# Kernel tuning notes

Measured on AMD Instinct MI355X. Metric: run time of the kernel, lower is better.

The kernel has to match this reference:

```python
import jax, jax.numpy as jnp
import numpy as np

B, S, D_IN, D_OUT, H = 2, 2048, 1024, 1024, 16
HD = D_OUT // H  # head dim = 64


def setup_inputs() -> dict:
    key = jax.random.key(0)
    ks = jax.random.split(key, 9)
    s_in = 1.0 / np.sqrt(D_IN)
    s_out = 1.0 / np.sqrt(D_OUT)
    return {
        "X": jax.random.normal(ks[0], (B, S, D_IN), dtype=jnp.float32),
        "Wq": jax.random.uniform(ks[1], (D_OUT, D_IN), jnp.float32, -s_in, s_in),
        "bq": jax.random.uniform(ks[2], (D_OUT,), jnp.float32, -s_in, s_in),
        "Wk": jax.random.uniform(ks[3], (D_OUT, D_IN), jnp.float32, -s_in, s_in),
        "bk": jax.random.uniform(ks[4], (D_OUT,), jnp.float32, -s_in, s_in),
        "Wv": jax.random.uniform(ks[5], (D_OUT, D_IN), jnp.float32, -s_in, s_in),
        "bv": jax.random.uniform(ks[6], (D_OUT,), jnp.float32, -s_in, s_in),
        "Wo": jax.random.uniform(ks[7], (D_OUT, D_OUT), jnp.float32, -s_out, s_out),
        "bo": jax.random.uniform(ks[8], (D_OUT,), jnp.float32, -s_out, s_out),
    }


def reference(X, Wq, bq, Wk, bk, Wv, bv, Wo, bo):
    scale = jnp.asarray(HD ** 0.5, X.dtype)  # self.dim = sqrt(head_dim)
    q = X @ Wq.T + bq  # [B,S,D_OUT]
    k = X @ Wk.T + bk
    v = X @ Wv.T + bv
    # split heads: b s (h d) -> b h s d
    q = q.reshape(B, S, H, HD).transpose(0, 2, 1, 3)
    k = k.reshape(B, S, H, HD).transpose(0, 2, 1, 3)
    v = v.reshape(B, S, H, HD).transpose(0, 2, 1, 3)
    scores = jnp.einsum('bhsd,bhtd->bhst', q, k) / scale  # [B,H,S,S]
    causal = jnp.triu(jnp.ones((S, S), dtype=bool), k=1)
    scores = jnp.where(causal, -jnp.inf, scores)
    weights = jax.nn.softmax(scores, axis=-1)
    out = jnp.einsum('bhst,bhtd->bhsd', weights, v)  # [B,H,S,HD]
    out = out.transpose(0, 2, 1, 3).reshape(B, S, D_OUT)  # b h s d -> b s (h d)
    return out @ Wo.T + bo
```

## Files before the change

### kernel.cpp

```cpp
#include <hip/hip_runtime.h>
#include <hip/hip_bf16.h>

typedef __bf16 bf16_t;
typedef __bf16 bf16x8 __attribute__((ext_vector_type(8)));
typedef float  f32x4  __attribute__((ext_vector_type(4)));
typedef unsigned short ushort_t;

#define MFMA16(a, b, c) __builtin_amdgcn_mfma_f32_16x16x32_bf16((a), (b), (c), 0, 0, 0)
#define GLDS16(g, l) __builtin_amdgcn_global_load_lds( \
    (const __attribute__((address_space(1))) unsigned int*)(g), \
    (__attribute__((address_space(3))) unsigned int*)(l), 16, 0, 0)

#define WAITCNT_VM(n)  (0x0F70 | (n))
#define WAITCNT_LGKM0  0xC07F

#define MEMFENCE asm volatile("" ::: "memory")

#define QSCALE 0.18033688f

__global__ __launch_bounds__(256) void cvt_all(
    const void* __restrict__ X,  const void* __restrict__ W0, const void* __restrict__ W1,
    const void* __restrict__ W2, const void* __restrict__ W3,
    const void* __restrict__ c0, const void* __restrict__ c1,
    const void* __restrict__ c2, const void* __restrict__ c3,
    bf16_t* __restrict__ Xb, bf16_t* __restrict__ Wb, float* __restrict__ biasF,
    int* __restrict__ flag)
{
    const int tid  = threadIdx.x;
    const int lane = tid & 63;
    const ushort_t u = ((const ushort_t*)X)[2 * lane];
    const int e = (u >> 7) & 0xFF;
    const int f = (__ballot(e >= 0xA0) != 0ull) ? 1 : 0;

    const int bid = blockIdx.x;
    if (bid >= 4096) {
        if (bid == 4096 && tid == 0) *flag = f;
        const int idx = ((bid - 4096) * 256 + tid) * 8;
        const int w = idx >> 10, off = idx & 1023;
        const void* src = (w == 0) ? c0 : (w == 1) ? c1 : (w == 2) ? c2 : c3;
        #pragma unroll
        for (int r = 0; r < 8; ++r)
            biasF[idx + r] = f ? ((const float*)src)[off + r]
                               : (float)((const bf16_t*)src)[off + r];
        return;
    }

    const long long i = (long long)bid * 2048 + tid * 8;
    const void* src;
    bf16_t* dst;
    long long off;
    if (i < 4194304) { src = X; dst = Xb; off = i; }
    else {
        const int w = (int)((i - 4194304) >> 20);
        off = (i - 4194304) & 1048575;
        src = (w == 0) ? W0 : (w == 1) ? W1 : (w == 2) ? W2 : W3;
        dst = Wb + (size_t)w * 1048576;
    }
    if (f) {
        const float* s = (const float*)src + off;
        const float4 a = *(const float4*)(s);
        const float4 b = *(const float4*)(s + 4);
        bf16x8 o;
        o[0] = (bf16_t)a.x; o[1] = (bf16_t)a.y; o[2] = (bf16_t)a.z; o[3] = (bf16_t)a.w;
        o[4] = (bf16_t)b.x; o[5] = (bf16_t)b.y; o[6] = (bf16_t)b.z; o[7] = (bf16_t)b.w;
        *(bf16x8*)(dst + off) = o;
    } else {
        *(bf16x8*)(dst + off) = *(const bf16x8*)((const bf16_t*)src + off);
    }
}

__global__ __launch_bounds__(512, 2) void gemm256(
    const bf16_t* __restrict__ A,
    const bf16_t* __restrict__ W0, const bf16_t* __restrict__ W1, const bf16_t* __restrict__ W2,
    const float* __restrict__ b0, const float* __restrict__ b1, const float* __restrict__ b2,
    bf16_t* __restrict__ C, bf16_t* __restrict__ Vt)
{
    __shared__ bf16_t Ash[4][256 * 32];
    __shared__ bf16_t Bsh[4][256 * 32];

    const int tid  = threadIdx.x;
    const int wid  = tid >> 6;
    const int lane = tid & 63;
    const int g    = lane >> 4;
    const int c    = lane & 15;

    const int m0  = blockIdx.x * 256;
    const int n0  = blockIdx.y * 256;
    const int mat = n0 >> 10;
    const bf16_t* W  = (mat == 0) ? W0 : (mat == 1) ? W1 : W2;
    const float*  bs = (mat == 0) ? b0 : (mat == 1) ? b1 : b2;
    const int nw = n0 & 1023;

    const int srow = lane >> 2;
    const int sblk = (lane & 3) ^ ((lane >> 3) & 3);
    const bf16_t* Ag = A + (size_t)(m0 + wid * 32 + srow) * 1024 + sblk * 8;
    const bf16_t* Wg = W + (size_t)(nw + wid * 32 + srow) * 1024 + sblk * 8;

    const int waveM = (wid >> 2) * 128;
    const int waveN = (wid & 3) * 64;
    const int fblk  = (g ^ ((c >> 1) & 3)) * 8;

    f32x4 acc[8][4] = {};

    auto stageA = [&](int H, int q) {
        GLDS16(Ag + (size_t)(q * 16) * 1024 + H * 32, &Ash[H & 3][(wid * 32 + q * 16) * 32]);
    };
    auto stageB = [&](int H, int q) {
        GLDS16(Wg + (size_t)(q * 16) * 1024 + H * 32, &Bsh[H & 3][(wid * 32 + q * 16) * 32]);
    };

    for (int H = 0; H < 3; ++H) {
        stageA(H, 0); stageA(H, 1); stageB(H, 0); stageB(H, 1);
    }
    __builtin_amdgcn_s_waitcnt(WAITCNT_VM(8));
    __builtin_amdgcn_s_barrier();
    MEMFENCE;

    #pragma unroll 1
    for (int H = 0; H < 32; ++H) {
        const int buf = H & 3;
        const bf16_t* As = Ash[buf];
        const bf16_t* Bs = Bsh[buf];
        const bool pre = (H + 3 < 32);

        bf16x8 bfr[4], af[4];
        #pragma unroll
        for (int j = 0; j < 4; ++j)
            bfr[j] = *(const bf16x8*)(&Bs[(waveN + j * 16 + c) * 32 + fblk]);
        #pragma unroll
        for (int i = 0; i < 4; ++i)
            af[i] = *(const bf16x8*)(&As[(waveM + i * 16 + c) * 32 + fblk]);
        if (pre) { stageA(H + 3, 0); stageB(H + 3, 0); }
        MEMFENCE;
        __builtin_amdgcn_s_barrier();
        __builtin_amdgcn_s_waitcnt(WAITCNT_LGKM0);
        __builtin_amdgcn_sched_barrier(0);
        __builtin_amdgcn_s_setprio(1);
        #pragma unroll
        for (int i = 0; i < 4; ++i)
            #pragma unroll
            for (int j = 0; j < 4; ++j)
                acc[i][j] = MFMA16(af[i], bfr[j], acc[i][j]);
        __builtin_amdgcn_s_setprio(0);
        MEMFENCE;
        __builtin_amdgcn_s_barrier();
        MEMFENCE;

        #pragma unroll
        for (int i = 0; i < 4; ++i)
            af[i] = *(const bf16x8*)(&As[(waveM + (i + 4) * 16 + c) * 32 + fblk]);
        if (pre) { stageA(H + 3, 1); stageB(H + 3, 1); }
        MEMFENCE;
        __builtin_amdgcn_s_barrier();
        __builtin_amdgcn_s_waitcnt(WAITCNT_LGKM0);
        __builtin_amdgcn_sched_barrier(0);
        __builtin_amdgcn_s_setprio(1);
        #pragma unroll
        for (int i = 0; i < 4; ++i)
            #pragma unroll
            for (int j = 0; j < 4; ++j)
                acc[i + 4][j] = MFMA16(af[i], bfr[j], acc[i + 4][j]);
        __builtin_amdgcn_s_setprio(0);
        MEMFENCE;
        if (H < 29)       __builtin_amdgcn_s_waitcnt(WAITCNT_VM(8));
        else if (H == 29) __builtin_amdgcn_s_waitcnt(WAITCNT_VM(4));
        else if (H == 30) __builtin_amdgcn_s_waitcnt(WAITCNT_VM(0));
        __builtin_amdgcn_s_barrier();
        MEMFENCE;
    }

    if (mat == 2) {
        #pragma unroll
        for (int j = 0; j < 4; ++j) {
            const int col  = n0 + waveN + j * 16 + c;
            const int hcol = col & 1023;
            const float bv = bs[hcol];
            const int h = hcol >> 6, d = hcol & 63;
            #pragma unroll
            for (int i = 0; i < 8; ++i) {
                const int row = m0 + waveM + i * 16 + g * 4;
                const int bb = row >> 11, s = row & 2047;
                bf16_t pk[4];
                #pragma unroll
                for (int r = 0; r < 4; ++r) pk[r] = (bf16_t)(acc[i][j][r] + bv);
                *(uint2*)(&Vt[(((size_t)bb * 16 + h) * 64 + d) * 2048 + s]) = *(uint2*)pk;
            }
        }
        return;
    }

    const float os = (mat == 0) ? QSCALE : 1.0f;
    #pragma unroll
    for (int j = 0; j < 4; ++j) {
        const int col = n0 + waveN + j * 16 + c;
        const float bv = bs[col & 1023];
        #pragma unroll
        for (int i = 0; i < 8; ++i) {
            const int row = m0 + waveM + i * 16 + g * 4;
            #pragma unroll
            for (int r = 0; r < 4; ++r)
                C[(size_t)(row + r) * 3072 + col] = (bf16_t)((acc[i][j][r] + bv) * os);
        }
    }
}

template<int TM>
__global__ __launch_bounds__(256, 2) void gemm_nt(
    const bf16_t* __restrict__ A,
    const bf16_t* __restrict__ W0, const bf16_t* __restrict__ W1, const bf16_t* __restrict__ W2,
    const float* __restrict__ b0, const float* __restrict__ b1, const float* __restrict__ b2,
    void* __restrict__ C, int ldc, bf16_t* __restrict__ Vt, int fuse_vt,
    const int* __restrict__ flag, int is_out)
{
    constexpr int MI = TM / 32;
    constexpr int G  = (TM == 128) ? 4 : 3;
    __shared__ bf16_t Ash[3][TM * 32];
    __shared__ bf16_t Bsh[3][128 * 32];

    const int f32out = is_out ? *flag : 0;

    const int tid  = threadIdx.x;
    const int wid  = tid >> 6;
    const int lane = tid & 63;
    const int g    = lane >> 4;
    const int c    = lane & 15;

    const int m0  = blockIdx.x * TM;
    const int n0  = blockIdx.y * 128;
    const int mat = n0 >> 10;
    const bf16_t* W  = (mat == 0) ? W0 : (mat == 1) ? W1 : W2;
    const float*  bs = (mat == 0) ? b0 : (mat == 1) ? b1 : b2;
    const int nw = n0 & 1023;

    const int srow = lane >> 2;
    const int sblk = (lane & 3) ^ ((lane >> 3) & 3);
    const bf16_t* Ag = A + (size_t)(m0 + wid * (TM / 4) + srow) * 1024 + sblk * 8;
    const bf16_t* Wg = W + (size_t)(nw + wid * 32 + srow) * 1024 + sblk * 8;

    const int waveM = (wid >> 1) * (TM / 2);
    const int waveN = (wid & 1) * 64;

    f32x4 acc[MI][4] = {};
    const int fblk = (g ^ ((c >> 1) & 3)) * 8;

    auto stage = [&](int t, int buf) {
        const int k0 = t * 32;
        bf16_t* As = &Ash[buf][(wid * (TM / 4)) * 32];
        bf16_t* Bs = &Bsh[buf][(wid * 32) * 32];
        GLDS16(Ag + k0, As);
        if (TM == 128) GLDS16(Ag + (size_t)16 * 1024 + k0, As + 16 * 32);
        GLDS16(Wg + k0, Bs);
        GLDS16(Wg + (size_t)16 * 1024 + k0, Bs + 16 * 32);
    };

    stage(0, 0);
    stage(1, 1);

    #pragma unroll 3
    for (int k = 0; k < 32; ++k) {
        if (k < 30) {
            stage(k + 2, (k + 2) % 3);
            __builtin_amdgcn_s_waitcnt(WAITCNT_VM(2 * G));
        } else if (k == 30) {
            __builtin_amdgcn_s_waitcnt(WAITCNT_VM(G));
        } else {
            __builtin_amdgcn_s_waitcnt(WAITCNT_VM(0));
        }
        __builtin_amdgcn_s_barrier();
        asm volatile("" ::: "memory");

        const int cur = k % 3;
        bf16x8 af[MI], bfr[4];
        #pragma unroll
        for (int i = 0; i < MI; ++i)
            af[i] = *(const bf16x8*)(&Ash[cur][(waveM + i * 16 + c) * 32 + fblk]);
        #pragma unroll
        for (int j = 0; j < 4; ++j)
            bfr[j] = *(const bf16x8*)(&Bsh[cur][(waveN + j * 16 + c) * 32 + fblk]);
        #pragma unroll
        for (int i = 0; i < MI; ++i)
            #pragma unroll
            for (int j = 0; j < 4; ++j)
                acc[i][j] = MFMA16(af[i], bfr[j], acc[i][j]);

        asm volatile("" ::: "memory");
        __builtin_amdgcn_s_waitcnt(WAITCNT_LGKM0);
        __builtin_amdgcn_s_barrier();
    }

    if (fuse_vt && mat == 2) {
        #pragma unroll
        for (int j = 0; j < 4; ++j) {
            const int col  = n0 + waveN + j * 16 + c;
            const int hcol = col & 1023;
            const float bv = bs[hcol];
            const int h = hcol >> 6, d = hcol & 63;
            #pragma unroll
            for (int i = 0; i < MI; ++i) {
                const int row = m0 + waveM + i * 16 + g * 4;
                const int bb = row >> 11, s = row & 2047;
                bf16_t pk[4];
                #pragma unroll
                for (int r = 0; r < 4; ++r) pk[r] = (bf16_t)(acc[i][j][r] + bv);
                *(uint2*)(&Vt[(((size_t)bb * 16 + h) * 64 + d) * 2048 + s]) = *(uint2*)pk;
            }
        }
        return;
    }

    const float oscale = (fuse_vt && mat == 0) ? QSCALE : 1.0f;
    #pragma unroll
    for (int j = 0; j < 4; ++j) {
        const int col = n0 + waveN + j * 16 + c;
        const float bv = bs[col & 1023];
        #pragma unroll
        for (int i = 0; i < MI; ++i) {
            const int row = m0 + waveM + i * 16 + g * 4;
            #pragma unroll
            for (int r = 0; r < 4; ++r) {
                const float val = (acc[i][j][r] + bv) * oscale;
                const size_t idx = (size_t)(row + r) * ldc + col;
                if (f32out) ((float*)C)[idx] = val;
                else        ((bf16_t*)C)[idx] = (bf16_t)val;
            }
        }
    }
}

__global__ __launch_bounds__(256, 4) void attn_kernel(
    const bf16_t* __restrict__ QKV, const bf16_t* __restrict__ Vt,
    bf16_t* __restrict__ O)
{
    __shared__ bf16_t Ksh[64][72];
    __shared__ bf16_t Vsh[64][72];
    __shared__ bf16_t Psh[4][16][72];

    const int tid  = threadIdx.x;
    const int wid  = tid >> 6;
    const int lane = tid & 63;
    const int g    = lane >> 4;
    const int c    = lane & 15;

    const int bh = blockIdx.y;
    const int b  = bh >> 4, h = bh & 15;
    const int qt = (bh < 16) ? blockIdx.x : (31 - blockIdx.x);
    const int q0 = qt * 64;
    const int nt = qt + 1;

    bf16x8 aq[2];
    {
        const bf16_t* qp = QKV + (size_t)(b * 2048 + q0 + wid * 16 + c) * 3072 + h * 64;
        aq[0] = *(const bf16x8*)(qp + g * 8);
        aq[1] = *(const bf16x8*)(qp + 32 + g * 8);
    }

    float li[4] = {};
    f32x4 o[4]  = {};

    const int sr  = tid >> 2;
    const int sc0 = (tid & 3) * 16;
    const bf16_t* Kg = QKV + (size_t)(b * 2048 + sr) * 3072 + 1024 + h * 64 + sc0;
    const bf16_t* Vg = Vt + ((size_t)bh * 64 + sr) * 2048 + sc0;

    uint4 kr0 = *(const uint4*)(Kg);
    uint4 kr1 = *(const uint4*)(Kg + 8);
    uint4 vr0 = *(const uint4*)(Vg);
    uint4 vr1 = *(const uint4*)(Vg + 8);

    for (int jt = 0; jt < nt; ++jt) {
        *(uint4*)(&Ksh[sr][sc0])     = kr0;
        *(uint4*)(&Ksh[sr][sc0 + 8]) = kr1;
        *(uint4*)(&Vsh[sr][sc0])     = vr0;
        *(uint4*)(&Vsh[sr][sc0 + 8]) = vr1;
        __syncthreads();

        if (jt + 1 < nt) {
            const size_t ko = (size_t)(jt + 1) * 64 * 3072;
            kr0 = *(const uint4*)(Kg + ko);
            kr1 = *(const uint4*)(Kg + ko + 8);
            vr0 = *(const uint4*)(Vg + (jt + 1) * 64);
            vr1 = *(const uint4*)(Vg + (jt + 1) * 64 + 8);
        }

        f32x4 s[4] = {};
        #pragma unroll
        for (int n = 0; n < 4; ++n)
            #pragma unroll
            for (int kb = 0; kb < 2; ++kb) {
                const bf16x8 kf = *(const bf16x8*)(&Ksh[n * 16 + c][kb * 32 + g * 8]);
                s[n] = MFMA16(aq[kb], kf, s[n]);
            }

        if (jt == nt - 1) {
            const int j0 = jt * 64;
            const int qrow = q0 + wid * 16 + g * 4;
            #pragma unroll
            for (int n = 0; n < 4; ++n)
                #pragma unroll
                for (int r = 0; r < 4; ++r)
                    if (j0 + n * 16 + c > qrow + r) s[n][r] = -1e30f;
        }

        #pragma unroll
        for (int n = 0; n < 4; ++n)
            #pragma unroll
            for (int r = 0; r < 4; ++r) {
                const float p = __builtin_amdgcn_exp2f(s[n][r]);
                li[r] += p;
                Psh[wid][g * 4 + r][n * 16 + c] = (bf16_t)p;
            }
        __builtin_amdgcn_wave_barrier();

        #pragma unroll
        for (int kb = 0; kb < 2; ++kb) {
            const bf16x8 ap = *(const bf16x8*)(&Psh[wid][c][kb * 32 + g * 8]);
            #pragma unroll
            for (int d = 0; d < 4; ++d) {
                const bf16x8 vf = *(const bf16x8*)(&Vsh[d * 16 + c][kb * 32 + g * 8]);
                o[d] = MFMA16(ap, vf, o[d]);
            }
        }
        __syncthreads();
    }

    #pragma unroll
    for (int off = 1; off < 16; off <<= 1)
        #pragma unroll
        for (int r = 0; r < 4; ++r)
            li[r] += __shfl_xor(li[r], off, 64);

    const int orow = b * 2048 + q0 + wid * 16 + g * 4;
    #pragma unroll
    for (int r = 0; r < 4; ++r) {
        const float inv = 1.0f / li[r];
        #pragma unroll
        for (int d = 0; d < 4; ++d)
            O[(size_t)(orow + r) * 1024 + h * 64 + d * 16 + c] = (bf16_t)(o[d][r] * inv);
    }
}

extern "C" void kernel_launch(void* const* d_in, const int* in_sizes, int n_in,
                              void* d_out, int out_size, void* d_ws, size_t ws_size,
                              hipStream_t stream)
{
    const void* X  = d_in[0];
    const void* Wq = d_in[1];  const void* bq = d_in[2];
    const void* Wk = d_in[3];  const void* bk = d_in[4];
    const void* Wv = d_in[5];  const void* bv = d_in[6];
    const void* Wo = d_in[7];  const void* bo = d_in[8];

    int*    flag  = (int*)d_ws;
    float*  biasF = (float*)((char*)d_ws + 16);
    bf16_t* Xb    = (bf16_t*)((char*)d_ws + 16 + 16384);
    bf16_t* Wb    = Xb  + (size_t)4096 * 1024;
    bf16_t* QKV   = Wb  + (size_t)4 * 1024 * 1024;
    bf16_t* Vt    = QKV + (size_t)4096 * 3072;
    bf16_t* Ao    = Vt  + (size_t)4096 * 1024;

    const size_t MW = (size_t)1024 * 1024;

    cvt_all<<<4098, 256, 0, stream>>>(X, Wq, Wk, Wv, Wo, bq, bk, bv, bo,
                                      Xb, Wb, biasF, flag);

    gemm256<<<dim3(16, 12), 512, 0, stream>>>(
        Xb, Wb, Wb + MW, Wb + 2 * MW,
        biasF, biasF + 1024, biasF + 2048, QKV, Vt);
    attn_kernel<<<dim3(32, 32), 256, 0, stream>>>(QKV, Vt, Ao);
    gemm_nt<64><<<dim3(64, 8), 256, 0, stream>>>(
        Ao, Wb + 3 * MW, Wb + 3 * MW, Wb + 3 * MW,
        biasF + 3072, biasF + 3072, biasF + 3072, d_out, 1024, (bf16_t*)nullptr, 0, flag, 1);
}
```

Before: 202.1 us.

## Collapse GEMM main loops to a single barrier per k-step

The 256x128 projection GEMM loop previously split each k-step into two half-phases, each with its own barriers. It now loads all eight A fragments at once, issues all four prefetches, and runs 32 MFMAs per barrier, with the loop unrolled by four. The smaller GEMM now issues its next-stage global-to-LDS copy after the fragment reads instead of before the barrier, and waits on memory only at the end of the iteration, so each k-step needs one barrier. The aim is to cut barrier stalls and let global loads overlap with MFMA work. The cost is higher register pressure from holding eight A fragments, plus reliance on exact vmcnt accounting across the multi-buffered LDS rings.

```diff
diff --git a/kernel.cpp b/kernel.cpp
--- a/kernel.cpp
+++ b/kernel.cpp
@@ -116,52 +116,32 @@
     __builtin_amdgcn_s_barrier();
     MEMFENCE;
 
-    #pragma unroll 1
+    #pragma unroll 4
     for (int H = 0; H < 32; ++H) {
         const int buf = H & 3;
         const bf16_t* As = Ash[buf];
         const bf16_t* Bs = Bsh[buf];
-        const bool pre = (H + 3 < 32);
-
-        bf16x8 bfr[4], af[4];
+
+        bf16x8 bfr[4], af[8];
         #pragma unroll
         for (int j = 0; j < 4; ++j)
             bfr[j] = *(const bf16x8*)(&Bs[(waveN + j * 16 + c) * 32 + fblk]);
         #pragma unroll
-        for (int i = 0; i < 4; ++i)
+        for (int i = 0; i < 8; ++i)
             af[i] = *(const bf16x8*)(&As[(waveM + i * 16 + c) * 32 + fblk]);
-        if (pre) { stageA(H + 3, 0); stageB(H + 3, 0); }
-        MEMFENCE;
-        __builtin_amdgcn_s_barrier();
-        __builtin_amdgcn_s_waitcnt(WAITCNT_LGKM0);
-        __builtin_amdgcn_sched_barrier(0);
+
+        if (H < 29) { stageA(H + 3, 0); stageA(H + 3, 1); stageB(H + 3, 0); stageB(H + 3, 1); }
+
         __builtin_amdgcn_s_setprio(1);
         #pragma unroll
-        for (int i = 0; i < 4; ++i)
+        for (int i = 0; i < 8; ++i)
             #pragma unroll
             for (int j = 0; j < 4; ++j)
                 acc[i][j] = MFMA16(af[i], bfr[j], acc[i][j]);
         __builtin_amdgcn_s_setprio(0);
+
         MEMFENCE;
-        __builtin_amdgcn_s_barrier();
-        MEMFENCE;
-
-        #pragma unroll
-        for (int i = 0; i < 4; ++i)
-            af[i] = *(const bf16x8*)(&As[(waveM + (i + 4) * 16 + c) * 32 + fblk]);
-        if (pre) { stageA(H + 3, 1); stageB(H + 3, 1); }
-        MEMFENCE;
-        __builtin_amdgcn_s_barrier();
         __builtin_amdgcn_s_waitcnt(WAITCNT_LGKM0);
-        __builtin_amdgcn_sched_barrier(0);
-        __builtin_amdgcn_s_setprio(1);
-        #pragma unroll
-        for (int i = 0; i < 4; ++i)
-            #pragma unroll
-            for (int j = 0; j < 4; ++j)
-                acc[i + 4][j] = MFMA16(af[i], bfr[j], acc[i + 4][j]);
-        __builtin_amdgcn_s_setprio(0);
-        MEMFENCE;
         if (H < 29)       __builtin_amdgcn_s_waitcnt(WAITCNT_VM(8));
         else if (H == 29) __builtin_amdgcn_s_waitcnt(WAITCNT_VM(4));
         else if (H == 30) __builtin_amdgcn_s_waitcnt(WAITCNT_VM(0));
@@ -255,20 +235,12 @@
 
     stage(0, 0);
     stage(1, 1);
+    __builtin_amdgcn_s_waitcnt(WAITCNT_VM(G));
+    __builtin_amdgcn_s_barrier();
+    MEMFENCE;
 
     #pragma unroll 3
     for (int k = 0; k < 32; ++k) {
-        if (k < 30) {
-            stage(k + 2, (k + 2) % 3);
-            __builtin_amdgcn_s_waitcnt(WAITCNT_VM(2 * G));
-        } else if (k == 30) {
-            __builtin_amdgcn_s_waitcnt(WAITCNT_VM(G));
-        } else {
-            __builtin_amdgcn_s_waitcnt(WAITCNT_VM(0));
-        }
-        __builtin_amdgcn_s_barrier();
-        asm volatile("" ::: "memory");
-
         const int cur = k % 3;
         bf16x8 af[MI], bfr[4];
         #pragma unroll
@@ -277,15 +249,21 @@
         #pragma unroll
         for (int j = 0; j < 4; ++j)
             bfr[j] = *(const bf16x8*)(&Bsh[cur][(waveN + j * 16 + c) * 32 + fblk]);
+
+        if (k < 30) stage(k + 2, (k + 2) % 3);
+
         #pragma unroll
         for (int i = 0; i < MI; ++i)
             #pragma unroll
             for (int j = 0; j < 4; ++j)
                 acc[i][j] = MFMA16(af[i], bfr[j], acc[i][j]);
 
-        asm volatile("" ::: "memory");
+        MEMFENCE;
         __builtin_amdgcn_s_waitcnt(WAITCNT_LGKM0);
+        if (k < 30)       __builtin_amdgcn_s_waitcnt(WAITCNT_VM(G));
+        else if (k == 30) __builtin_amdgcn_s_waitcnt(WAITCNT_VM(0));
         __builtin_amdgcn_s_barrier();
+        MEMFENCE;
     }
 
     if (fuse_vt && mat == 2) {
```

Result: faster. 197.8 us (-2.1%).
